# Optimization experiments

Hardware: AMD Instinct MI355X
Metric: run time of the kernel (lower is better)

The kernel has to match this reference:

```python
import jax, jax.numpy as jnp
import numpy as np

N_NODES = 100000
N_EDGES = 1600000
N_FEAT = 128
N_CLASSES = 64
K_HOPS = 2


def setup_inputs() -> dict:
    key = jax.random.key(0)
    k1, k2, k3 = jax.random.split(key, 3)
    x = jax.random.normal(k1, (N_NODES, N_FEAT), dtype=jnp.float32)
    edge_index = jax.random.randint(k2, (2, N_EDGES), 0, N_NODES, dtype=jnp.int64)
    # Linear layer params (PyG Linear: y = x @ W.T + b)
    lim = 1.0 / np.sqrt(N_FEAT)
    W = jax.random.uniform(k3, (N_CLASSES, N_FEAT), dtype=jnp.float32, minval=-lim, maxval=lim)
    b = jnp.zeros((N_CLASSES,), dtype=jnp.float32)
    return {"x": x, "edge_index": edge_index, "W": W, "b": b}


def _gcn_norm(edge_index, num_nodes):
    # Add self-loops with weight 1 (PyG gcn_norm default)
    loops = jnp.arange(num_nodes, dtype=edge_index.dtype)
    row = jnp.concatenate([edge_index[0], loops])
    col = jnp.concatenate([edge_index[1], loops])
    ew = jnp.ones(row.shape[0], dtype=jnp.float32)
    deg = jax.ops.segment_sum(ew, col, num_segments=num_nodes)
    dinv = jnp.where(deg > 0, jax.lax.rsqrt(deg), 0.0)
    norm = dinv[row] * ew * dinv[col]  # [E + N]
    return row, col, norm


def reference(x, edge_index, W, b):
    n = x.shape[0]
    row, col, norm = _gcn_norm(edge_index, n)
    # K rounds of normalized SpMM: out[col] += norm * x[row]
    for _ in range(K_HOPS):
        x = jax.ops.segment_sum(norm[:, None] * x[row], col, num_segments=n)
    # Final linear
    return x @ W.T + b
```

## Files before the change

### kernel.cpp

```cpp
#include <hip/hip_runtime.h>
#include <hip/hip_fp16.h>

#define NFEAT 128
#define NCLS  64
#define CPB   192
#define NBMAX 1024
#define PCHUNK 8192
#define HGRID 256

__global__ __launch_bounds__(256) void hist_k(const int* __restrict__ col, int E,
                                              int* __restrict__ bhist,
                                              int* __restrict__ done,
                                              int* __restrict__ bptr,
                                              int* __restrict__ bcursor, int NB) {
    __shared__ int h[NBMAX];
    __shared__ int sc[256];
    __shared__ int lastf;
    int t = threadIdx.x;
    for (int i = t; i < NB; i += 256) h[i] = 0;
    __syncthreads();
    int stride = gridDim.x * 256;
    for (int e = blockIdx.x * 256 + t; e < E; e += stride)
        atomicAdd(&h[col[e] / CPB], 1);
    __syncthreads();
    for (int i = t; i < NB; i += 256)
        if (h[i]) atomicAdd(&bhist[i], h[i]);
    __threadfence();
    if (t == 0) {
        int old = atomicAdd(done, 1);
        lastf = (old == HGRID - 1);
    }
    __syncthreads();
    if (!lastf) return;

    int v[4]; int base = t * 4;
#pragma unroll
    for (int k = 0; k < 4; ++k) {
        int i = base + k;
        v[k] = (i < NB) ? bhist[i] : 0;
    }
    int tot = v[0] + v[1] + v[2] + v[3];
    sc[t] = tot;
    for (int off = 1; off < 256; off <<= 1) {
        __syncthreads();
        int a = (t >= off) ? sc[t - off] : 0;
        __syncthreads();
        sc[t] += a;
    }
    __syncthreads();
    int off = sc[t] - tot;
    int run = 0;
#pragma unroll
    for (int k = 0; k < 4; ++k) {
        int i = base + k;
        if (i < NB) { int p = off + run; bptr[i] = p; bcursor[i] = p; }
        run += v[k];
    }
    if (t == 255) bptr[NB] = sc[255];
}

__global__ __launch_bounds__(256) void part_k(const int* __restrict__ row,
                                              const int* __restrict__ col, int E,
                                              int* __restrict__ bcursor,
                                              int* __restrict__ ebuf, int NB) {
    __shared__ int h[NBMAX];
    __shared__ int cur[NBMAX];
    int t = threadIdx.x;
    int start = blockIdx.x * PCHUNK;
    int end   = min(start + PCHUNK, E);
    for (int i = t; i < NB; i += 256) h[i] = 0;
    __syncthreads();
    for (int e = start + t; e < end; e += 256)
        atomicAdd(&h[col[e] / CPB], 1);
    __syncthreads();
    for (int i = t; i < NB; i += 256)
        cur[i] = h[i] ? atomicAdd(&bcursor[i], h[i]) : 0;
    __syncthreads();
    for (int e = start + t; e < end; e += 256) {
        int c = col[e], b = c / CPB, cl = c - b * CPB;
        int pos = atomicAdd(&cur[b], 1);
        ebuf[pos] = row[e] | (cl << 17);
    }
}

__global__ __launch_bounds__(256) void sort_k(const int* __restrict__ ebuf,
                                              const int* __restrict__ bptr,
                                              float* __restrict__ dinv,
                                              int* __restrict__ ptrv, int* __restrict__ cnt,
                                              int* __restrict__ csr, int N) {
    __shared__ int h[CPB];
    __shared__ int cur[CPB];
    __shared__ int sc[256];
    int b = blockIdx.x, t = threadIdx.x;
    for (int i = t; i < CPB; i += 256) h[i] = 0;
    __syncthreads();
    int s = bptr[b], e = bptr[b + 1];
    for (int j = s + t; j < e; j += 256)
        atomicAdd(&h[ebuf[j] >> 17], 1);
    __syncthreads();
    int v = (t < CPB) ? h[t] : 0;
    sc[t] = v;
    for (int off = 1; off < 256; off <<= 1) {
        __syncthreads();
        int a = (t >= off) ? sc[t - off] : 0;
        __syncthreads();
        sc[t] += a;
    }
    __syncthreads();
    if (t < CPB) {
        int c = b * CPB + t;
        int p = s + sc[t] - v;
        cur[t] = p;
        if (c < N) {
            ptrv[c] = p; cnt[c] = v;
            dinv[c] = rsqrtf((float)(v + 1));
        }
    }
    __syncthreads();
    for (int j = s + t; j < e; j += 256) {
        int p = ebuf[j];
        int pos = atomicAdd(&cur[p >> 17], 1);
        csr[pos] = p & 0x1FFFF;
    }
}

__global__ __launch_bounds__(256) void proj_k(const float* __restrict__ x,
                                              const float* __restrict__ W,
                                              const float* __restrict__ dinv,
                                              __half* __restrict__ z, int n) {
    __shared__ float xs[64][132];
    __shared__ float ws[128][68];
    int t = threadIdx.x;
    int nb = blockIdx.x * 64;

    for (int it = 0; it < 8; ++it) {
        int chunk = t + it * 256;
        int c  = chunk >> 5;
        int f4 = (chunk & 31) << 2;
        float4 wv = *reinterpret_cast<const float4*>(&W[c * NFEAT + f4]);
        ws[f4 + 0][c] = wv.x; ws[f4 + 1][c] = wv.y;
        ws[f4 + 2][c] = wv.z; ws[f4 + 3][c] = wv.w;
    }
    for (int it = 0; it < 8; ++it) {
        int chunk = t + it * 256;
        int nloc = chunk >> 5;
        int f4   = (chunk & 31) << 2;
        int g = nb + nloc;
        float4 xv = (g < n) ? *reinterpret_cast<const float4*>(&x[(size_t)g * NFEAT + f4])
                            : make_float4(0.f, 0.f, 0.f, 0.f);
        *reinterpret_cast<float4*>(&xs[nloc][f4]) = xv;
    }
    __syncthreads();

    int tc = t & 15;
    int tn = t >> 4;
    float4 acc[4];
#pragma unroll
    for (int i = 0; i < 4; ++i) acc[i] = make_float4(0.f, 0.f, 0.f, 0.f);

    for (int f4 = 0; f4 < NFEAT; f4 += 4) {
        float4 xv[4], wv[4];
#pragma unroll
        for (int i = 0; i < 4; ++i)
            xv[i] = *reinterpret_cast<const float4*>(&xs[tn + 16 * i][f4]);
#pragma unroll
        for (int k = 0; k < 4; ++k)
            wv[k] = *reinterpret_cast<const float4*>(&ws[f4 + k][tc * 4]);
#pragma unroll
        for (int i = 0; i < 4; ++i) {
            acc[i].x += xv[i].x * wv[0].x + xv[i].y * wv[1].x + xv[i].z * wv[2].x + xv[i].w * wv[3].x;
            acc[i].y += xv[i].x * wv[0].y + xv[i].y * wv[1].y + xv[i].z * wv[2].y + xv[i].w * wv[3].y;
            acc[i].z += xv[i].x * wv[0].z + xv[i].y * wv[1].z + xv[i].z * wv[2].z + xv[i].w * wv[3].z;
            acc[i].w += xv[i].x * wv[0].w + xv[i].y * wv[1].w + xv[i].z * wv[2].w + xv[i].w * wv[3].w;
        }
    }
#pragma unroll
    for (int i = 0; i < 4; ++i) {
        int g = nb + tn + 16 * i;
        if (g < n) {
            float d = dinv[g];
            __half2 h0 = __floats2half2_rn(acc[i].x * d, acc[i].y * d);
            __half2 h1 = __floats2half2_rn(acc[i].z * d, acc[i].w * d);
            uint2 pk;
            pk.x = *reinterpret_cast<unsigned int*>(&h0);
            pk.y = *reinterpret_cast<unsigned int*>(&h1);
            *reinterpret_cast<uint2*>(&z[(size_t)g * NCLS + tc * 4]) = pk;
        }
    }
}

template <int FINAL>
__global__ __launch_bounds__(256) void spmm_k(const __half* __restrict__ zin,
                                              void* __restrict__ outp,
                                              const int* __restrict__ ptrv,
                                              const int* __restrict__ cnt,
                                              const float* __restrict__ dinv,
                                              const int* __restrict__ csr,
                                              const float* __restrict__ bias, int n) {
    int t = threadIdx.x;
    int lane = t & 63;
    int wid  = blockIdx.x * 4 + (t >> 6);
    wid = __builtin_amdgcn_readfirstlane(wid);
    if (wid >= n) return;

    int sub = lane >> 3;
    int cg  = (lane & 7) * 8;
    int s = ptrv[wid];
    int e = s + cnt[wid];

    float a[8];
#pragma unroll
    for (int k = 0; k < 8; ++k) a[k] = 0.f;

#define ACCUM(u)                                                            \
    {                                                                       \
        __half2 t0 = *reinterpret_cast<const __half2*>(&u.x);               \
        __half2 t1 = *reinterpret_cast<const __half2*>(&u.y);               \
        __half2 t2 = *reinterpret_cast<const __half2*>(&u.z);               \
        __half2 t3 = *reinterpret_cast<const __half2*>(&u.w);               \
        float2 f0 = __half22float2(t0), f1 = __half22float2(t1);            \
        float2 f2 = __half22float2(t2), f3 = __half22float2(t3);            \
        a[0] += f0.x; a[1] += f0.y; a[2] += f1.x; a[3] += f1.y;             \
        a[4] += f2.x; a[5] += f2.y; a[6] += f3.x; a[7] += f3.y;             \
    }

    int j = s;
    for (; j + 16 <= e; j += 16) {
        int r0 = csr[j + sub];
        int r1 = csr[j + 8 + sub];
        uint4 g0 = *reinterpret_cast<const uint4*>(&zin[(size_t)r0 * NCLS + cg]);
        uint4 g1 = *reinterpret_cast<const uint4*>(&zin[(size_t)r1 * NCLS + cg]);
        ACCUM(g0); ACCUM(g1);
    }
    if (j + 8 <= e) {
        int r0 = csr[j + sub];
        uint4 g0 = *reinterpret_cast<const uint4*>(&zin[(size_t)r0 * NCLS + cg]);
        ACCUM(g0);
        j += 8;
    }
    if (j + sub < e) {
        int r0 = csr[j + sub];
        uint4 g0 = *reinterpret_cast<const uint4*>(&zin[(size_t)r0 * NCLS + cg]);
        ACCUM(g0);
    }

#pragma unroll
    for (int m = 8; m <= 32; m <<= 1)
#pragma unroll
        for (int k = 0; k < 8; ++k)
            a[k] += __shfl_xor(a[k], m, 64);

    uint4 sv = *reinterpret_cast<const uint4*>(&zin[(size_t)wid * NCLS + cg]);
    ACCUM(sv);
#undef ACCUM

    float d = dinv[wid];
    if (FINAL) {
        float* out = (float*)outp;
        float4 b0 = *reinterpret_cast<const float4*>(&bias[cg]);
        float4 b1 = *reinterpret_cast<const float4*>(&bias[cg + 4]);
        if (sub == 0) {
            float4 o0, o1;
            o0.x = fmaf(d, a[0], b0.x); o0.y = fmaf(d, a[1], b0.y);
            o0.z = fmaf(d, a[2], b0.z); o0.w = fmaf(d, a[3], b0.w);
            o1.x = fmaf(d, a[4], b1.x); o1.y = fmaf(d, a[5], b1.y);
            o1.z = fmaf(d, a[6], b1.z); o1.w = fmaf(d, a[7], b1.w);
            *reinterpret_cast<float4*>(&out[(size_t)wid * NCLS + cg])     = o0;
            *reinterpret_cast<float4*>(&out[(size_t)wid * NCLS + cg + 4]) = o1;
        }
    } else {
        __half* zo = (__half*)outp;
        float d2 = d * d;
        if (sub == 0) {
            __half2 h0 = __floats2half2_rn(d2 * a[0], d2 * a[1]);
            __half2 h1 = __floats2half2_rn(d2 * a[2], d2 * a[3]);
            __half2 h2 = __floats2half2_rn(d2 * a[4], d2 * a[5]);
            __half2 h3 = __floats2half2_rn(d2 * a[6], d2 * a[7]);
            uint4 pk;
            pk.x = *reinterpret_cast<unsigned int*>(&h0);
            pk.y = *reinterpret_cast<unsigned int*>(&h1);
            pk.z = *reinterpret_cast<unsigned int*>(&h2);
            pk.w = *reinterpret_cast<unsigned int*>(&h3);
            *reinterpret_cast<uint4*>(&zo[(size_t)wid * NCLS + cg]) = pk;
        }
    }
}

extern "C" void kernel_launch(void* const* d_in, const int* in_sizes, int n_in,
                              void* d_out, int out_size, void* d_ws, size_t ws_size,
                              hipStream_t stream) {
    const float* x  = (const float*)d_in[0];
    const int*   ei = (const int*)d_in[1];
    const float* W  = (const float*)d_in[2];
    const float* b  = (const float*)d_in[3];

    const int N = in_sizes[0] / NFEAT;
    const int E = in_sizes[1] / 2;
    const int* row = ei;
    const int* col = ei + E;
    const int NB = (N + CPB - 1) / CPB;
    if (NB + 1 > NBMAX) return;

    __half* z0     = (__half*)d_ws;
    __half* z1     = z0 + (size_t)N * NCLS;
    int*   ebuf    = (int*)(z1 + (size_t)N * NCLS);
    int*   csr     = ebuf + E;
    float* dinv    = (float*)(csr + E);
    int*   ptrv    = (int*)(dinv + N);
    int*   cnt     = ptrv + N;
    int*   bhist   = cnt + N;
    int*   done    = bhist + NB;
    int*   bptr    = done + 1;
    int*   bcursor = bptr + NB + 1;

    size_t needed = (size_t)N * NCLS * 2 * 2
                  + ((size_t)E * 2 + (size_t)N * 3 + 3 * (size_t)NB + 2) * 4;
    if (ws_size < needed) return;

    hipMemsetAsync(bhist, 0, ((size_t)NB + 1) * 4, stream);
    hist_k<<<HGRID, 256, 0, stream>>>(col, E, bhist, done, bptr, bcursor, NB);
    part_k<<<(E + PCHUNK - 1) / PCHUNK, 256, 0, stream>>>(row, col, E, bcursor, ebuf, NB);
    sort_k<<<NB, 256, 0, stream>>>(ebuf, bptr, dinv, ptrv, cnt, csr, N);

    proj_k<<<(N + 63) / 64, 256, 0, stream>>>(x, W, dinv, z0, N);

    spmm_k<0><<<(N + 3) / 4, 256, 0, stream>>>(z0, (void*)z1,  ptrv, cnt, dinv, csr, b, N);
    spmm_k<1><<<(N + 3) / 4, 256, 0, stream>>>(z1, d_out,      ptrv, cnt, dinv, csr, b, N);
}
```

Before: 290.6 us.

## Use MFMA fp16 matrix cores for projection and retune partition grid sizes

Rewrites the dense projection kernel to compute x@W.T with 16x16x32 fp16 MFMA instructions instead of fp32 FMA from shared-memory tiles. Weight fragments are loaded directly into registers per wave and results are staged through a small LDS buffer for coalesced 16-byte stores. It also halves the partition chunk size and doubles the histogram grid. The inputs are now rounded to fp16 before the multiply, which lowers precision. The LDS staging relies on s_waitcnt with no barrier, which is only safe because each wave touches only its own slice.

```diff
diff --git a/kernel.cpp b/kernel.cpp
--- a/kernel.cpp
+++ b/kernel.cpp
@@ -5,8 +5,12 @@
 #define NCLS  64
 #define CPB   192
 #define NBMAX 1024
-#define PCHUNK 8192
-#define HGRID 256
+#define PCHUNK 4096
+#define HGRID 512
+
+typedef _Float16 f16;
+typedef __attribute__((ext_vector_type(8))) _Float16 f16x8;
+typedef __attribute__((ext_vector_type(4))) float f32x4;
 
 __global__ __launch_bounds__(256) void hist_k(const int* __restrict__ col, int E,
                                               int* __restrict__ bhist,
@@ -127,65 +131,71 @@
 __global__ __launch_bounds__(256) void proj_k(const float* __restrict__ x,
                                               const float* __restrict__ W,
                                               const float* __restrict__ dinv,
-                                              __half* __restrict__ z, int n) {
-    __shared__ float xs[64][132];
-    __shared__ float ws[128][68];
+                                              f16* __restrict__ z, int n) {
+    __shared__ __align__(16) f16 zbuf[4][16][64];
     int t = threadIdx.x;
-    int nb = blockIdx.x * 64;
-
-    for (int it = 0; it < 8; ++it) {
-        int chunk = t + it * 256;
-        int c  = chunk >> 5;
-        int f4 = (chunk & 31) << 2;
-        float4 wv = *reinterpret_cast<const float4*>(&W[c * NFEAT + f4]);
-        ws[f4 + 0][c] = wv.x; ws[f4 + 1][c] = wv.y;
-        ws[f4 + 2][c] = wv.z; ws[f4 + 3][c] = wv.w;
-    }
-    for (int it = 0; it < 8; ++it) {
-        int chunk = t + it * 256;
-        int nloc = chunk >> 5;
-        int f4   = (chunk & 31) << 2;
-        int g = nb + nloc;
-        float4 xv = (g < n) ? *reinterpret_cast<const float4*>(&x[(size_t)g * NFEAT + f4])
-                            : make_float4(0.f, 0.f, 0.f, 0.f);
-        *reinterpret_cast<float4*>(&xs[nloc][f4]) = xv;
-    }
-    __syncthreads();
-
-    int tc = t & 15;
-    int tn = t >> 4;
-    float4 acc[4];
-#pragma unroll
-    for (int i = 0; i < 4; ++i) acc[i] = make_float4(0.f, 0.f, 0.f, 0.f);
-
-    for (int f4 = 0; f4 < NFEAT; f4 += 4) {
-        float4 xv[4], wv[4];
-#pragma unroll
-        for (int i = 0; i < 4; ++i)
-            xv[i] = *reinterpret_cast<const float4*>(&xs[tn + 16 * i][f4]);
-#pragma unroll
-        for (int k = 0; k < 4; ++k)
-            wv[k] = *reinterpret_cast<const float4*>(&ws[f4 + k][tc * 4]);
-#pragma unroll
-        for (int i = 0; i < 4; ++i) {
-            acc[i].x += xv[i].x * wv[0].x + xv[i].y * wv[1].x + xv[i].z * wv[2].x + xv[i].w * wv[3].x;
-            acc[i].y += xv[i].x * wv[0].y + xv[i].y * wv[1].y + xv[i].z * wv[2].y + xv[i].w * wv[3].y;
-            acc[i].z += xv[i].x * wv[0].z + xv[i].y * wv[1].z + xv[i].z * wv[2].z + xv[i].w * wv[3].z;
-            acc[i].w += xv[i].x * wv[0].w + xv[i].y * wv[1].w + xv[i].z * wv[2].w + xv[i].w * wv[3].w;
-        }
-    }
-#pragma unroll
-    for (int i = 0; i < 4; ++i) {
-        int g = nb + tn + 16 * i;
-        if (g < n) {
-            float d = dinv[g];
-            __half2 h0 = __floats2half2_rn(acc[i].x * d, acc[i].y * d);
-            __half2 h1 = __floats2half2_rn(acc[i].z * d, acc[i].w * d);
-            uint2 pk;
-            pk.x = *reinterpret_cast<unsigned int*>(&h0);
-            pk.y = *reinterpret_cast<unsigned int*>(&h1);
-            *reinterpret_cast<uint2*>(&z[(size_t)g * NCLS + tc * 4]) = pk;
-        }
+    int w = t >> 6, l = t & 63;
+    int lr = l & 15;
+    int lk = l >> 4;
+
+    f16x8 bfrag[4][4];
+#pragma unroll
+    for (int ct = 0; ct < 4; ++ct)
+#pragma unroll
+        for (int m = 0; m < 4; ++m) {
+            const float* wp = &W[(size_t)(ct * 16 + lr) * NFEAT + m * 32 + lk * 8];
+            float4 w0 = *reinterpret_cast<const float4*>(wp);
+            float4 w1 = *reinterpret_cast<const float4*>(wp + 4);
+            f16x8 bb;
+            bb[0] = (f16)w0.x; bb[1] = (f16)w0.y; bb[2] = (f16)w0.z; bb[3] = (f16)w0.w;
+            bb[4] = (f16)w1.x; bb[5] = (f16)w1.y; bb[6] = (f16)w1.z; bb[7] = (f16)w1.w;
+            bfrag[ct][m] = bb;
+        }
+
+    int nb = blockIdx.x * 64 + w * 16;
+    int arow = nb + lr;
+    bool aok = arow < n;
+    const float* xp = &x[(size_t)(aok ? arow : 0) * NFEAT + lk * 8];
+
+    f32x4 acc[4];
+#pragma unroll
+    for (int ct = 0; ct < 4; ++ct) acc[ct] = (f32x4){0.f, 0.f, 0.f, 0.f};
+
+#pragma unroll
+    for (int m = 0; m < 4; ++m) {
+        float4 x0 = make_float4(0.f, 0.f, 0.f, 0.f);
+        float4 x1 = make_float4(0.f, 0.f, 0.f, 0.f);
+        if (aok) {
+            x0 = *reinterpret_cast<const float4*>(xp + m * 32);
+            x1 = *reinterpret_cast<const float4*>(xp + m * 32 + 4);
+        }
+        f16x8 a;
+        a[0] = (f16)x0.x; a[1] = (f16)x0.y; a[2] = (f16)x0.z; a[3] = (f16)x0.w;
+        a[4] = (f16)x1.x; a[5] = (f16)x1.y; a[6] = (f16)x1.z; a[7] = (f16)x1.w;
+#pragma unroll
+        for (int ct = 0; ct < 4; ++ct)
+            acc[ct] = __builtin_amdgcn_mfma_f32_16x16x32_f16(a, bfrag[ct][m], acc[ct], 0, 0, 0);
+    }
+
+    float d[4];
+#pragma unroll
+    for (int r = 0; r < 4; ++r) {
+        int node = nb + lk * 4 + r;
+        d[r] = (node < n) ? dinv[node] : 0.f;
+    }
+#pragma unroll
+    for (int ct = 0; ct < 4; ++ct)
+#pragma unroll
+        for (int r = 0; r < 4; ++r)
+            zbuf[w][lk * 4 + r][ct * 16 + lr] = (f16)(acc[ct][r] * d[r]);
+    __builtin_amdgcn_s_waitcnt(0);
+
+    const uint4* zb = reinterpret_cast<const uint4*>(&zbuf[w][0][0]);
+    uint4 v0 = zb[l * 2], v1 = zb[l * 2 + 1];
+    int node = nb + (l >> 2);
+    if (node < n) {
+        uint4* op = reinterpret_cast<uint4*>(&z[(size_t)node * NCLS + (l & 3) * 16]);
+        op[0] = v0; op[1] = v1;
     }
 }
 
@@ -301,8 +311,8 @@
     const int NB = (N + CPB - 1) / CPB;
     if (NB + 1 > NBMAX) return;
 
-    __half* z0     = (__half*)d_ws;
-    __half* z1     = z0 + (size_t)N * NCLS;
+    f16*   z0      = (f16*)d_ws;
+    f16*   z1      = z0 + (size_t)N * NCLS;
     int*   ebuf    = (int*)(z1 + (size_t)N * NCLS);
     int*   csr     = ebuf + E;
     float* dinv    = (float*)(csr + E);
@@ -324,6 +334,6 @@
 
     proj_k<<<(N + 63) / 64, 256, 0, stream>>>(x, W, dinv, z0, N);
 
-    spmm_k<0><<<(N + 3) / 4, 256, 0, stream>>>(z0, (void*)z1,  ptrv, cnt, dinv, csr, b, N);
-    spmm_k<1><<<(N + 3) / 4, 256, 0, stream>>>(z1, d_out,      ptrv, cnt, dinv, csr, b, N);
-}
+    spmm_k<0><<<(N + 3) / 4, 256, 0, stream>>>((const __half*)z0, (void*)z1, ptrv, cnt, dinv, csr, b, N);
+    spmm_k<1><<<(N + 3) / 4, 256, 0, stream>>>((const __half*)z1, d_out,     ptrv, cnt, dinv, csr, b, N);
+}
```

Result: no change. 293.5 us (+1.0%).
